# Performance work log

Hardware: AMD Instinct MI355X
Metric: run time of the kernel (lower is better)

The kernel has to match this reference:

```python
import jax, jax.numpy as jnp
import numpy as np

B, S, D, H, E, K = 2, 1024, 768, 12, 8, 2
DF = 4 * D
HD = D // H
EPS = 1e-5

def layer_norm(x, g, b):
    m = jnp.mean(x, axis=-1, keepdims=True)
    v = jnp.mean(jnp.square(x - m), axis=-1, keepdims=True)
    return (x - m) * jax.lax.rsqrt(v + EPS) * g + b

def setup_inputs() -> dict:
    key = jax.random.key(0)
    ks = jax.random.split(key, 16)
    s = lambda i, shape, sc: jax.random.normal(ks[i], shape, jnp.float32) * sc
    return {
        'x': s(0, (B, S, D), 1.0),
        'ln1_g': jnp.ones((D,), jnp.float32), 'ln1_b': jnp.zeros((D,), jnp.float32),
        'Wq': s(1, (D, D), 0.02), 'Wk': s(2, (D, D), 0.02), 'Wv': s(3, (D, D), 0.02),
        'Wo': s(4, (D, D), 0.02), 'bo': jnp.zeros((D,), jnp.float32),
        'ln2_g': jnp.ones((D,), jnp.float32), 'ln2_b': jnp.zeros((D,), jnp.float32),
        'Wr': s(5, (D, E), 0.02), 'br': jnp.zeros((E,), jnp.float32),
        'W1': s(6, (E, D, DF), 0.02), 'b1': jnp.zeros((E, DF), jnp.float32),
        'W2': s(7, (E, DF, D), 0.02), 'b2': jnp.zeros((E, D), jnp.float32),
    }

def _attn(xn, Wq, Wk, Wv, Wo, bo):
    # xn: [B,S,D]
    q = (xn @ Wq).reshape(B, S, H, HD).transpose(0, 2, 1, 3)
    k = (xn @ Wk).reshape(B, S, H, HD).transpose(0, 2, 1, 3)
    v = (xn @ Wv).reshape(B, S, H, HD).transpose(0, 2, 1, 3)
    scores = jnp.einsum('bhqd,bhkd->bhqk', q, k) / jnp.sqrt(jnp.float32(HD))
    causal = jnp.tril(jnp.ones((S, S), bool))
    scores = jnp.where(causal, scores, jnp.float32(-1e9))
    w = jax.nn.softmax(scores, axis=-1)
    out = jnp.einsum('bhqk,bhkd->bhqd', w, v)
    out = out.transpose(0, 2, 1, 3).reshape(B, S, D)
    return out @ Wo + bo

def _smoe(xn, Wr, br, W1, b1, W2, b2):
    logits = xn @ Wr + br                               # [B,S,E]
    topv, topi = jax.lax.top_k(logits, K)               # [B,S,K]
    gw = jax.nn.softmax(topv, axis=-1)                  # softmax over selected experts
    oh = jax.nn.one_hot(topi, E, dtype=xn.dtype)        # [B,S,K,E]
    gate = jnp.einsum('bske,bsk->bse', oh, gw)          # sparse gate, zeros elsewhere
    h = jax.nn.gelu(jnp.einsum('bsd,edf->bsef', xn, W1) + b1, approximate=False)
    eo = jnp.einsum('bsef,efd->bsed', h, W2) + b2       # [B,S,E,D]
    return jnp.einsum('bsed,bse->bsd', eo, gate)

def reference(x, ln1_g, ln1_b, Wq, Wk, Wv, Wo, bo, ln2_g, ln2_b, Wr, br, W1, b1, W2, b2):
    h = x + _attn(layer_norm(x, ln1_g, ln1_b), Wq, Wk, Wv, Wo, bo)
    out = h + _smoe(layer_norm(h, ln2_g, ln2_b), Wr, br, W1, b1, W2, b2)
    return out
```

## Files before the change

### kernel.cpp

```cpp
#include <hip/hip_runtime.h>

using bf16x8 = __attribute__((ext_vector_type(8))) short;
using bf16x4 = __attribute__((ext_vector_type(4))) short;
using f32x4  = __attribute__((ext_vector_type(4))) float;

#define DEV __device__ __forceinline__

DEV short f2bf(float x){
  unsigned u = __float_as_uint(x);
  u += 0x7fffu + ((u >> 16) & 1u);
  return (short)(u >> 16);
}
DEV float bf2f(short h){ return __uint_as_float(((unsigned)(unsigned short)h) << 16); }

#define MFMA16(a,b,c) __builtin_amdgcn_mfma_f32_16x16x32_bf16(a,b,c,0,0,0)

DEV void gl_lds16(const void* g, void* l){
  __builtin_amdgcn_global_load_lds(
      (const __attribute__((address_space(1))) unsigned*)g,
      (__attribute__((address_space(3))) unsigned*)l, 16, 0, 0);
}


__global__ void k_transpose(const float* __restrict__ src, long sbatch,
                            short* __restrict__ dhi, short* __restrict__ dlo, long dbatch,
                            int R, int C){
  __shared__ float tile[64][65];
  const float* s = src + (long)blockIdx.z * sbatch;
  int c0 = blockIdx.x * 64, r0 = blockIdx.y * 64;
  int tx = threadIdx.x & 15, ty = threadIdx.x >> 4;
  #pragma unroll
  for (int i = 0; i < 4; i++){
    int r = ty + 16*i;
    float4 v = *(const float4*)&s[(long)(r0 + r) * C + c0 + tx*4];
    tile[r][tx*4+0] = v.x; tile[r][tx*4+1] = v.y;
    tile[r][tx*4+2] = v.z; tile[r][tx*4+3] = v.w;
  }
  __syncthreads();
  int rseg = (threadIdx.x & 7) * 8;
  #pragma unroll
  for (int p = 0; p < 2; p++){
    int col = (threadIdx.x >> 3) + 32*p;
    short hv[8], lv[8];
    #pragma unroll
    for (int k = 0; k < 8; k++){
      float v = tile[rseg + k][col];
      hv[k] = f2bf(v);
      lv[k] = f2bf(v - bf2f(hv[k]));
    }
    long o = (long)blockIdx.z * dbatch + (long)(c0 + col) * R + r0 + rseg;
    *(bf16x8*)&dhi[o] = *(bf16x8*)&hv[0];
    if (dlo) *(bf16x8*)&dlo[o] = *(bf16x8*)&lv[0];
  }
}

__global__ void k_transpose4(const float* __restrict__ s0, const float* __restrict__ s1,
                             const float* __restrict__ s2, const float* __restrict__ s3,
                             short* __restrict__ d0h, short* __restrict__ d0l,
                             short* __restrict__ d1h, short* __restrict__ d1l,
                             short* __restrict__ d2h, short* __restrict__ d2l,
                             short* __restrict__ d3h, short* __restrict__ d3l){
  int z = blockIdx.z;
  const float* s = (z==0) ? s0 : (z==1) ? s1 : (z==2) ? s2 : s3;
  short* dh = (z==0) ? d0h : (z==1) ? d1h : (z==2) ? d2h : d3h;
  short* dl = (z==0) ? d0l : (z==1) ? d1l : (z==2) ? d2l : d3l;
  __shared__ float tile[64][65];
  int c0 = blockIdx.x * 64, r0 = blockIdx.y * 64;
  int tx = threadIdx.x & 15, ty = threadIdx.x >> 4;
  #pragma unroll
  for (int i = 0; i < 4; i++){
    int r = ty + 16*i;
    float4 v = *(const float4*)&s[(long)(r0 + r) * 768 + c0 + tx*4];
    tile[r][tx*4+0] = v.x; tile[r][tx*4+1] = v.y;
    tile[r][tx*4+2] = v.z; tile[r][tx*4+3] = v.w;
  }
  __syncthreads();
  int rseg = (threadIdx.x & 7) * 8;
  #pragma unroll
  for (int p = 0; p < 2; p++){
    int col = (threadIdx.x >> 3) + 32*p;
    short hv[8], lv[8];
    #pragma unroll
    for (int k = 0; k < 8; k++){
      float v = tile[rseg + k][col];
      hv[k] = f2bf(v);
      lv[k] = f2bf(v - bf2f(hv[k]));
    }
    long o = (long)(c0 + col) * 768 + r0 + rseg;
    *(bf16x8*)&dh[o] = *(bf16x8*)&hv[0];
    *(bf16x8*)&dl[o] = *(bf16x8*)&lv[0];
  }
}

__global__ void k_ln1(const float* __restrict__ x, const float* __restrict__ g,
                      const float* __restrict__ bb,
                      short* __restrict__ xh, short* __restrict__ xl){
  int t = blockIdx.x, tid = threadIdx.x;
  const float* xr = x + (long)t * 768;
  float v[3];
  #pragma unroll
  for (int j = 0; j < 3; j++) v[j] = xr[tid + 256*j];
  float s = v[0]+v[1]+v[2];
  float q = v[0]*v[0]+v[1]*v[1]+v[2]*v[2];
  #pragma unroll
  for (int o = 32; o > 0; o >>= 1){ s += __shfl_down(s,o,64); q += __shfl_down(q,o,64); }
  __shared__ float ss[4], qs[4];
  int w = tid >> 6;
  if ((tid & 63) == 0){ ss[w] = s; qs[w] = q; }
  __syncthreads();
  float St = ss[0]+ss[1]+ss[2]+ss[3], Qt = qs[0]+qs[1]+qs[2]+qs[3];
  float mean = St * (1.f/768.f);
  float var  = Qt * (1.f/768.f) - mean*mean;
  float inv  = 1.f / sqrtf(var + 1e-5f);
  #pragma unroll
  for (int j = 0; j < 3; j++){
    int d = tid + 256*j;
    float xn = (v[j]-mean)*inv*g[d] + bb[d];
    short hv = f2bf(xn);
    xh[(long)t*768 + d] = hv;
    xl[(long)t*768 + d] = f2bf(xn - bf2f(hv));
  }
}

__global__ __launch_bounds__(256,3) void k_qkv(
    const short* __restrict__ Ah, const short* __restrict__ Al,
    const short* __restrict__ Bh, const short* __restrict__ Bl,
    short* __restrict__ qh, short* __restrict__ ql,
    short* __restrict__ kh, short* __restrict__ kl,
    short* __restrict__ vh, short* __restrict__ vl){
  int M0 = blockIdx.x * 64, N0 = blockIdx.y * 128;
  __shared__ __align__(16) short lah[64*64], lal[64*64], lbh[128*64], lbl[128*64];
  int tid = threadIdx.x;
  int w = tid >> 6, lane = tid & 63, l15 = lane & 15, quad = lane >> 4;
  int mbase = (w & 1) * 32, nbase = (w >> 1) * 64;
  f32x4 acc[2][4];
  #pragma unroll
  for (int i = 0; i < 2; i++)
    #pragma unroll
    for (int j = 0; j < 4; j++) acc[i][j] = (f32x4){0.f,0.f,0.f,0.f};
  int rl = lane >> 3, pch = lane & 7;
  long gA[2], gB[4];
  #pragma unroll
  for (int j = 0; j < 2; j++){
    int r = w*16 + j*8 + rl;
    int c = pch ^ (r & 7);
    gA[j] = (long)(M0 + r)*768 + c*8;
  }
  #pragma unroll
  for (int j = 0; j < 4; j++){
    int r = w*32 + j*8 + rl;
    int c = pch ^ (r & 7);
    gB[j] = (long)(N0 + r)*768 + c*8;
  }
  for (int k0 = 0; k0 < 768; k0 += 64){
    #pragma unroll
    for (int j = 0; j < 2; j++){
      gl_lds16(Ah + gA[j] + k0, lah + w*1024 + j*512);
      gl_lds16(Al + gA[j] + k0, lal + w*1024 + j*512);
    }
    #pragma unroll
    for (int j = 0; j < 4; j++){
      gl_lds16(Bh + gB[j] + k0, lbh + w*2048 + j*512);
      gl_lds16(Bl + gB[j] + k0, lbl + w*2048 + j*512);
    }
    __syncthreads();
    #pragma unroll
    for (int kk = 0; kk < 2; kk++){
      int swq = ((kk*4 + quad) ^ (l15 & 7)) * 8;
      bf16x8 afh[2], afl[2];
      #pragma unroll
      for (int mt = 0; mt < 2; mt++){
        afh[mt] = *(const bf16x8*)&lah[(mbase+mt*16+l15)*64 + swq];
        afl[mt] = *(const bf16x8*)&lal[(mbase+mt*16+l15)*64 + swq];
      }
      #pragma unroll
      for (int nt = 0; nt < 4; nt++){
        bf16x8 bfh = *(const bf16x8*)&lbh[(nbase+nt*16+l15)*64 + swq];
        bf16x8 bfl = *(const bf16x8*)&lbl[(nbase+nt*16+l15)*64 + swq];
        #pragma unroll
        for (int mt = 0; mt < 2; mt++){
          acc[mt][nt] = MFMA16(afh[mt], bfh, acc[mt][nt]);
          acc[mt][nt] = MFMA16(afh[mt], bfl, acc[mt][nt]);
          acc[mt][nt] = MFMA16(afl[mt], bfh, acc[mt][nt]);
        }
      }
    }
    __syncthreads();
  }
  #pragma unroll
  for (int mt = 0; mt < 2; mt++){
    #pragma unroll
    for (int nt = 0; nt < 4; nt++){
      #pragma unroll
      for (int rg = 0; rg < 4; rg++){
        int m = M0 + mbase + mt*16 + quad*4 + rg;
        int n = N0 + nbase + nt*16 + l15;
        float vv = acc[mt][nt][rg];
        int bi = m >> 10, si = m & 1023;
        if (n < 768){
          float sv = vv * 0.18033688011112042f;
          short hv = f2bf(sv);
          int hh = n >> 6, hd = n & 63;
          long o = (((long)(bi*12+hh)*1024) + si)*64 + hd;
          qh[o] = hv; ql[o] = f2bf(sv - bf2f(hv));
        } else if (n < 1536){
          int n2 = n - 768;
          short hv = f2bf(vv);
          int hh = n2 >> 6, hd = n2 & 63;
          long o = (((long)(bi*12+hh)*1024) + si)*64 + hd;
          kh[o] = hv; kl[o] = f2bf(vv - bf2f(hv));
        } else {
          int n2 = n - 1536;
          short hv = f2bf(vv);
          int hh = n2 >> 6, hd = n2 & 63;
          long o = (((long)(bi*12+hh)*64) + hd)*1024 + si;
          vh[o] = hv; vl[o] = f2bf(vv - bf2f(hv));
        }
      }
    }
  }
}

__global__ __launch_bounds__(256,3) void k_attn(
    const short* __restrict__ qh, const short* __restrict__ ql,
    const short* __restrict__ kh, const short* __restrict__ kl,
    const short* __restrict__ vth, const short* __restrict__ vtl,
    float* __restrict__ po, float* __restrict__ pm, float* __restrict__ pl){
  int wid = (blockIdx.x + 3*blockIdx.y) & 31;
  int qt = wid >> 1, half = wid & 1, bh = blockIdx.y;
  int q0 = qt * 64;
  long base = (long)bh * 1024 * 64;
  int ktb = half ? ((qt + 2) >> 1) : 0;
  int kte = half ? (qt + 1) : ((qt + 2) >> 1);
  __shared__ __align__(16) short skh[64*64], skl[64*64], svh[64*64], svl[64*64];
  __shared__ __align__(16) short sph[4][16*72], spl[4][16*72];
  int tid = threadIdx.x, w = tid >> 6, lane = tid & 63, l15 = lane & 15, quad = lane >> 4;
  bf16x8 qfh[2], qfl[2];
  #pragma unroll
  for (int c = 0; c < 2; c++){
    long qa = base + (long)(q0 + w*16 + l15)*64 + c*32 + quad*8;
    qfh[c] = *(const bf16x8*)(qh + qa);
    qfl[c] = *(const bf16x8*)(ql + qa);
  }
  f32x4 oacc[4];
  #pragma unroll
  for (int i = 0; i < 4; i++) oacc[i] = (f32x4){0.f,0.f,0.f,0.f};
  float m_i[4] = {-1e30f,-1e30f,-1e30f,-1e30f};
  float l_i[4] = {0.f,0.f,0.f,0.f};
  const short* gsrc = (w==0) ? kh : (w==1) ? kl : (w==2) ? vth : vtl;
  short* myb = (w==0) ? skh : (w==1) ? skl : (w==2) ? svh : svl;
  bool isv = (w >= 2);
  int rloc = lane >> 3, pch = lane & 7;
  for (int kt = ktb; kt < kte; kt++){
    #pragma unroll
    for (int j = 0; j < 8; j++){
      int r = j*8 + rloc;
      int c = pch ^ (r & 7);
      long ga = isv ? (base + (long)r*1024 + kt*64 + c*8)
                    : (base + (long)(kt*64 + r)*64 + c*8);
      gl_lds16(gsrc + ga, myb + j*512);
    }
    __syncthreads();
    f32x4 sfr[4];
    #pragma unroll
    for (int nt = 0; nt < 4; nt++){
      f32x4 c = (f32x4){0.f,0.f,0.f,0.f};
      int krow = (nt*16 + l15) * 64;
      #pragma unroll
      for (int ch = 0; ch < 2; ch++){
        int pc = ((ch*4 + quad) ^ (l15 & 7)) * 8;
        bf16x8 kfh = *(const bf16x8*)&skh[krow + pc];
        bf16x8 kfl = *(const bf16x8*)&skl[krow + pc];
        c = MFMA16(qfh[ch], kfh, c);
        c = MFMA16(qfh[ch], kfl, c);
        c = MFMA16(qfl[ch], kfh, c);
      }
      sfr[nt] = c;
    }
    if (kt == qt){
      #pragma unroll
      for (int nt = 0; nt < 4; nt++)
        #pragma unroll
        for (int rg = 0; rg < 4; rg++){
          int kp = nt*16 + l15, qp = w*16 + quad*4 + rg;
          if (kp > qp) sfr[nt][rg] = -1e30f;
        }
    }
    float rmax[4];
    #pragma unroll
    for (int rg = 0; rg < 4; rg++)
      rmax[rg] = fmaxf(fmaxf(sfr[0][rg], sfr[1][rg]), fmaxf(sfr[2][rg], sfr[3][rg]));
    #pragma unroll
    for (int xm = 1; xm < 16; xm <<= 1)
      #pragma unroll
      for (int rg = 0; rg < 4; rg++)
        rmax[rg] = fmaxf(rmax[rg], __shfl_xor(rmax[rg], xm, 64));
    float alpha[4];
    #pragma unroll
    for (int rg = 0; rg < 4; rg++){
      float mn = fmaxf(m_i[rg], rmax[rg]);
      alpha[rg] = exp2f(m_i[rg] - mn);
      m_i[rg] = mn;
    }
    float rsum[4] = {0.f,0.f,0.f,0.f};
    #pragma unroll
    for (int nt = 0; nt < 4; nt++)
      #pragma unroll
      for (int rg = 0; rg < 4; rg++){
        float p = exp2f(sfr[nt][rg] - m_i[rg]);
        sfr[nt][rg] = p; rsum[rg] += p;
      }
    #pragma unroll
    for (int xm = 1; xm < 16; xm <<= 1)
      #pragma unroll
      for (int rg = 0; rg < 4; rg++)
        rsum[rg] += __shfl_xor(rsum[rg], xm, 64);
    #pragma unroll
    for (int rg = 0; rg < 4; rg++) l_i[rg] = l_i[rg]*alpha[rg] + rsum[rg];
    #pragma unroll
    for (int hd = 0; hd < 4; hd++)
      #pragma unroll
      for (int rg = 0; rg < 4; rg++) oacc[hd][rg] *= alpha[rg];
    #pragma unroll
    for (int nt = 0; nt < 4; nt++)
      #pragma unroll
      for (int rg = 0; rg < 4; rg++){
        float p = sfr[nt][rg];
        short hv = f2bf(p);
        sph[w][(quad*4+rg)*72 + nt*16 + l15] = hv;
        spl[w][(quad*4+rg)*72 + nt*16 + l15] = f2bf(p - bf2f(hv));
      }
    bf16x8 pfh[2], pfl[2];
    #pragma unroll
    for (int ch = 0; ch < 2; ch++){
      pfh[ch] = *(const bf16x8*)&sph[w][l15*72 + ch*32 + quad*8];
      pfl[ch] = *(const bf16x8*)&spl[w][l15*72 + ch*32 + quad*8];
    }
    #pragma unroll
    for (int hd = 0; hd < 4; hd++){
      int vrow = (hd*16 + l15) * 64;
      #pragma unroll
      for (int ch = 0; ch < 2; ch++){
        int pc = ((ch*4 + quad) ^ (l15 & 7)) * 8;
        bf16x8 vfh = *(const bf16x8*)&svh[vrow + pc];
        bf16x8 vfl = *(const bf16x8*)&svl[vrow + pc];
        oacc[hd] = MFMA16(pfh[ch], vfh, oacc[hd]);
        oacc[hd] = MFMA16(pfh[ch], vfl, oacc[hd]);
        oacc[hd] = MFMA16(pfl[ch], vfh, oacc[hd]);
      }
    }
    __syncthreads();
  }
  long pb = ((long)(half*24 + bh)*1024);
  #pragma unroll
  for (int hdt = 0; hdt < 4; hdt++)
    #pragma unroll
    for (int rg = 0; rg < 4; rg++){
      int qp = q0 + w*16 + quad*4 + rg;
      po[(pb + qp)*64 + hdt*16 + l15] = oacc[hdt][rg];
    }
  if (l15 == 0){
    #pragma unroll
    for (int rg = 0; rg < 4; rg++){
      int qp = q0 + w*16 + quad*4 + rg;
      pm[pb + qp] = m_i[rg];
      pl[pb + qp] = l_i[rg];
    }
  }
}

__global__ void k_attn_combine(const float* __restrict__ po, const float* __restrict__ pm,
                               const float* __restrict__ pl,
                               short* __restrict__ oh, short* __restrict__ ol){
  int bh = blockIdx.y, tid = threadIdx.x;
  int r = blockIdx.x*64 + (tid >> 2);
  int c0 = (tid & 3) * 16;
  long i0 = (long)bh*1024 + r;
  long i1 = (long)(24 + bh)*1024 + r;
  float m0 = pm[i0], m1 = pm[i1], l0 = pl[i0], l1 = pl[i1];
  float m = fmaxf(m0, m1);
  float a0 = exp2f(m0 - m), a1 = exp2f(m1 - m);
  float inv = 1.f / (a0*l0 + a1*l1);
  a0 *= inv; a1 *= inv;
  int b = bh / 12, hh = bh % 12;
  long ob = ((long)(b*1024 + r))*768 + hh*64 + c0;
  short hv[16], lv[16];
  #pragma unroll
  for (int j = 0; j < 4; j++){
    float4 o0 = *(const float4*)&po[i0*64 + c0 + j*4];
    float4 o1 = *(const float4*)&po[i1*64 + c0 + j*4];
    float vs[4] = {a0*o0.x + a1*o1.x, a0*o0.y + a1*o1.y,
                   a0*o0.z + a1*o1.z, a0*o0.w + a1*o1.w};
    #pragma unroll
    for (int q = 0; q < 4; q++){
      short h = f2bf(vs[q]);
      hv[j*4+q] = h; lv[j*4+q] = f2bf(vs[q] - bf2f(h));
    }
  }
  *(bf16x8*)(oh + ob)     = *(bf16x8*)&hv[0];
  *(bf16x8*)(oh + ob + 8) = *(bf16x8*)&hv[8];
  *(bf16x8*)(ol + ob)     = *(bf16x8*)&lv[0];
  *(bf16x8*)(ol + ob + 8) = *(bf16x8*)&lv[8];
}

__global__ __launch_bounds__(256,3) void k_wo(
    const short* __restrict__ Ah, const short* __restrict__ Al,
    const short* __restrict__ Bh, const short* __restrict__ Bl,
    float* __restrict__ p0, float* __restrict__ p1){
  int M0 = blockIdx.x * 64, N0 = blockIdx.y * 128;
  int ks = blockIdx.z;
  int kbeg = ks * 384;
  float* wp = ks ? p1 : p0;
  __shared__ __align__(16) short lah[64*64], lal[64*64], lbh[128*64], lbl[128*64];
  int tid = threadIdx.x;
  int w = tid >> 6, lane = tid & 63, l15 = lane & 15, quad = lane >> 4;
  int mbase = (w & 1) * 32, nbase = (w >> 1) * 64;
  f32x4 acc[2][4];
  #pragma unroll
  for (int i = 0; i < 2; i++)
    #pragma unroll
    for (int j = 0; j < 4; j++) acc[i][j] = (f32x4){0.f,0.f,0.f,0.f};
  int rl = lane >> 3, pch = lane & 7;
  long gA[2], gB[4];
  #pragma unroll
  for (int j = 0; j < 2; j++){
    int r = w*16 + j*8 + rl;
    int c = pch ^ (r & 7);
    gA[j] = (long)(M0 + r)*768 + kbeg + c*8;
  }
  #pragma unroll
  for (int j = 0; j < 4; j++){
    int r = w*32 + j*8 + rl;
    int c = pch ^ (r & 7);
    gB[j] = (long)(N0 + r)*768 + kbeg + c*8;
  }
  for (int k0 = 0; k0 < 384; k0 += 64){
    #pragma unroll
    for (int j = 0; j < 2; j++){
      gl_lds16(Ah + gA[j] + k0, lah + w*1024 + j*512);
      gl_lds16(Al + gA[j] + k0, lal + w*1024 + j*512);
    }
    #pragma unroll
    for (int j = 0; j < 4; j++){
      gl_lds16(Bh + gB[j] + k0, lbh + w*2048 + j*512);
      gl_lds16(Bl + gB[j] + k0, lbl + w*2048 + j*512);
    }
    __syncthreads();
    #pragma unroll
    for (int kk = 0; kk < 2; kk++){
      int swq = ((kk*4 + quad) ^ (l15 & 7)) * 8;
      bf16x8 afh[2], afl[2];
      #pragma unroll
      for (int mt = 0; mt < 2; mt++){
        afh[mt] = *(const bf16x8*)&lah[(mbase+mt*16+l15)*64 + swq];
        afl[mt] = *(const bf16x8*)&lal[(mbase+mt*16+l15)*64 + swq];
      }
      #pragma unroll
      for (int nt = 0; nt < 4; nt++){
        bf16x8 bfh = *(const bf16x8*)&lbh[(nbase+nt*16+l15)*64 + swq];
        bf16x8 bfl = *(const bf16x8*)&lbl[(nbase+nt*16+l15)*64 + swq];
        #pragma unroll
        for (int mt = 0; mt < 2; mt++){
          acc[mt][nt] = MFMA16(afh[mt], bfh, acc[mt][nt]);
          acc[mt][nt] = MFMA16(afh[mt], bfl, acc[mt][nt]);
          acc[mt][nt] = MFMA16(afl[mt], bfh, acc[mt][nt]);
        }
      }
    }
    __syncthreads();
  }
  #pragma unroll
  for (int mt = 0; mt < 2; mt++)
    #pragma unroll
    for (int nt = 0; nt < 4; nt++)
      #pragma unroll
      for (int rg = 0; rg < 4; rg++){
        int m = M0 + mbase + mt*16 + quad*4 + rg;
        int n = N0 + nbase + nt*16 + l15;
        wp[(long)m*768 + n] = acc[mt][nt][rg];
      }
}

__global__ void k_ln2router(const float* __restrict__ p0, const float* __restrict__ p1,
                            const float* __restrict__ x, const float* __restrict__ bo,
                            const float* __restrict__ g, const float* __restrict__ bb,
                            const float* __restrict__ Wr, const float* __restrict__ br,
                            float* __restrict__ hout, short* __restrict__ xn2,
                            int* __restrict__ sel, float* __restrict__ gw){
  int wv = (blockIdx.x*256 + threadIdx.x) >> 6;
  int lane = threadIdx.x & 63;
  #pragma unroll
  for (int rep = 0; rep < 2; rep++){
    int t = wv*2 + rep;
    float4 hv[3];
    #pragma unroll
    for (int j = 0; j < 3; j++){
      long i = (long)t*192 + j*64 + lane;
      float4 a  = ((const float4*)p0)[i];
      float4 b  = ((const float4*)p1)[i];
      float4 xx = ((const float4*)x)[i];
      float4 bv = ((const float4*)bo)[j*64 + lane];
      float4 h;
      h.x = a.x + b.x + xx.x + bv.x;
      h.y = a.y + b.y + xx.y + bv.y;
      h.z = a.z + b.z + xx.z + bv.z;
      h.w = a.w + b.w + xx.w + bv.w;
      ((float4*)hout)[i] = h;
      hv[j] = h;
    }
    float s = 0.f, q = 0.f;
    #pragma unroll
    for (int j = 0; j < 3; j++){
      s += hv[j].x + hv[j].y + hv[j].z + hv[j].w;
      q += hv[j].x*hv[j].x + hv[j].y*hv[j].y + hv[j].z*hv[j].z + hv[j].w*hv[j].w;
    }
    #pragma unroll
    for (int xm = 1; xm < 64; xm <<= 1){ s += __shfl_xor(s, xm, 64); q += __shfl_xor(q, xm, 64); }
    float mean = s * (1.f/768.f);
    float var  = q * (1.f/768.f) - mean*mean;
    float inv  = 1.f / sqrtf(var + 1e-5f);
    float part[8] = {0,0,0,0,0,0,0,0};
    #pragma unroll
    for (int j = 0; j < 3; j++){
      int d0 = (j*64 + lane) * 4;
      float4 gv = ((const float4*)g)[j*64 + lane];
      float4 bbv = ((const float4*)bb)[j*64 + lane];
      float xn0 = (hv[j].x - mean)*inv*gv.x + bbv.x;
      float xn1 = (hv[j].y - mean)*inv*gv.y + bbv.y;
      float xn2v = (hv[j].z - mean)*inv*gv.z + bbv.z;
      float xn3 = (hv[j].w - mean)*inv*gv.w + bbv.w;
      bf16x4 pk = (bf16x4){f2bf(xn0), f2bf(xn1), f2bf(xn2v), f2bf(xn3)};
      *(bf16x4*)&xn2[(long)t*768 + d0] = pk;
      #pragma unroll
      for (int e = 0; e < 8; e++){
        part[e] += xn0 * Wr[(d0+0)*8 + e];
        part[e] += xn1 * Wr[(d0+1)*8 + e];
        part[e] += xn2v * Wr[(d0+2)*8 + e];
        part[e] += xn3 * Wr[(d0+3)*8 + e];
      }
    }
    #pragma unroll
    for (int xm = 1; xm < 64; xm <<= 1)
      #pragma unroll
      for (int e = 0; e < 8; e++) part[e] += __shfl_xor(part[e], xm, 64);
    if (lane == 0){
      float lg[8];
      #pragma unroll
      for (int e = 0; e < 8; e++) lg[e] = part[e] + br[e];
      int i1 = 0;
      for (int e = 1; e < 8; e++) if (lg[e] > lg[i1]) i1 = e;
      int i2 = -1;
      for (int e = 0; e < 8; e++){ if (e == i1) continue; if (i2 < 0 || lg[e] > lg[i2]) i2 = e; }
      float e2 = expf(lg[i2] - lg[i1]);
      float is = 1.f / (1.f + e2);
      gw[t*2]   = is;
      gw[t*2+1] = e2 * is;
      sel[t*2]   = i1;
      sel[t*2+1] = i2;
    }
  }
}

__global__ void k_build(const int* __restrict__ sel, int* __restrict__ poffs,
                        int* __restrict__ mbc, int* __restrict__ ptot,
                        int* __restrict__ pperm, int* __restrict__ inv){
  __shared__ int cnt8[8], cur[8], wbase[16][8];
  int tid = threadIdx.x;
  int lane = tid & 63, wv = tid >> 6;
  if (tid < 8) cnt8[tid] = 0;
  __syncthreads();
  int sv[4];
  #pragma unroll
  for (int r = 0; r < 4; r++){
    sv[r] = sel[tid + r*1024];
    #pragma unroll
    for (int e = 0; e < 8; e++){
      unsigned long long mk = __ballot(sv[r] == e);
      if (lane == 0) atomicAdd(&cnt8[e], (int)__popcll(mk));
    }
  }
  __syncthreads();
  if (tid == 0){
    int p = 0;
    for (int e = 0; e < 8; e++){
      cur[e] = p; poffs[e] = p;
      int pc = (cnt8[e] + 127) & ~127;
      mbc[e] = pc >> 7;
      p += pc;
    }
    *ptot = p;
  }
  __syncthreads();
  #pragma unroll
  for (int r = 0; r < 5; r++) pperm[tid + r*1024] = -1;
  __syncthreads();
  unsigned long long lmask = (1ull << lane) - 1ull;
  #pragma unroll
  for (int r = 0; r < 4; r++){
    int s = sv[r];
    unsigned long long mk[8];
    #pragma unroll
    for (int e = 0; e < 8; e++) mk[e] = __ballot(s == e);
    if (lane == 0){
      #pragma unroll
      for (int e = 0; e < 8; e++)
        wbase[wv][e] = atomicAdd(&cur[e], (int)__popcll(mk[e]));
    }
    unsigned long long mks = 0;
    #pragma unroll
    for (int e = 0; e < 8; e++) if (s == e) mks = mk[e];
    int pos = wbase[wv][s] + (int)__popcll(mks & lmask);
    int i = tid + r*1024;
    pperm[pos] = i;
    inv[i] = pos;
  }
}

__global__ __launch_bounds__(256,3) void k_moe1(
    const short* __restrict__ xn2, const short* __restrict__ W1T,
    const float* __restrict__ b1,
    const int* __restrict__ poffs, const int* __restrict__ mbc,
    const int* __restrict__ pperm, short* __restrict__ h1){
  int t = blockIdx.x;
  int e = t / 24, n = t % 24;
  if ((int)blockIdx.y >= mbc[e]) return;
  int M0 = poffs[e] + blockIdx.y * 128;
  int N0 = n * 128;
  const short* Bp = W1T + (long)e * 3072 * 768;
  __shared__ __align__(16) short la[128*64], lb[128*64];
  __shared__ int rtok[128];
  int tid = threadIdx.x, w = tid >> 6, lane = tid & 63, l15 = lane & 15, quad = lane >> 4;
  if (tid < 128) rtok[tid] = pperm[M0 + tid];
  __syncthreads();
  int rl = lane >> 3, pch = lane & 7;
  long gA[4], gB[4];
  #pragma unroll
  for (int j = 0; j < 4; j++){
    int r = w*32 + j*8 + rl;
    int c = pch ^ (r & 7);
    int tk = rtok[r]; tk = (tk >= 0) ? (tk >> 1) : 0;
    gA[j] = (long)tk*768 + c*8;
    gB[j] = (long)(N0 + r)*768 + c*8;
  }
  short* ldA = la + w*2048;
  short* ldB = lb + w*2048;
  f32x4 acc[4][4];
  #pragma unroll
  for (int i = 0; i < 4; i++)
    #pragma unroll
    for (int j = 0; j < 4; j++) acc[i][j] = (f32x4){0.f,0.f,0.f,0.f};
  int mbase = (w & 1) * 64, nbase = (w >> 1) * 64;
  for (int k0 = 0; k0 < 768; k0 += 64){
    #pragma unroll
    for (int j = 0; j < 4; j++) gl_lds16(xn2 + gA[j] + k0, ldA + j*512);
    #pragma unroll
    for (int j = 0; j < 4; j++) gl_lds16(Bp  + gB[j] + k0, ldB + j*512);
    __syncthreads();
    #pragma unroll
    for (int kk = 0; kk < 2; kk++){
      int swq = ((kk*4 + quad) ^ (l15 & 7)) * 8;
      bf16x8 af[4];
      #pragma unroll
      for (int mt = 0; mt < 4; mt++)
        af[mt] = *(const bf16x8*)&la[(mbase+mt*16+l15)*64 + swq];
      #pragma unroll
      for (int nt = 0; nt < 4; nt++){
        bf16x8 bf = *(const bf16x8*)&lb[(nbase+nt*16+l15)*64 + swq];
        #pragma unroll
        for (int mt = 0; mt < 4; mt++) acc[mt][nt] = MFMA16(af[mt], bf, acc[mt][nt]);
      }
    }
    __syncthreads();
  }
  #pragma unroll
  for (int mt = 0; mt < 4; mt++)
    #pragma unroll
    for (int nt = 0; nt < 4; nt++)
      #pragma unroll
      for (int rg = 0; rg < 4; rg++){
        int ml = mbase + mt*16 + quad*4 + rg;
        if (rtok[ml] >= 0){
          int nn = N0 + nbase + nt*16 + l15;
          float vv = acc[mt][nt][rg] + b1[e*3072 + nn];
          float gl = 0.5f * vv * (1.f + erff(vv * 0.70710678118654752f));
          h1[(long)(M0 + ml)*3072 + nn] = f2bf(gl);
        }
      }
}

__global__ __launch_bounds__(256,4) void k_moe2(
    const short* __restrict__ h1, const short* __restrict__ W2T,
    const float* __restrict__ b2,
    const int* __restrict__ poffs, const int* __restrict__ mbc,
    float* __restrict__ e0, float* __restrict__ e1,
    float* __restrict__ e2, float* __restrict__ e3){
  int t = blockIdx.x;
  int e = t / 24, r24 = t % 24;
  int n = r24 >> 2, ks = r24 & 3;
  if ((int)blockIdx.y >= mbc[e]) return;
  int M0 = poffs[e] + blockIdx.y * 128;
  int N0 = n * 128;
  int kbeg = ks * 768;
  const short* Bp = W2T + (long)e * 768 * 3072;
  float* eo = (ks == 0) ? e0 : (ks == 1) ? e1 : (ks == 2) ? e2 : e3;
  __shared__ __align__(16) short la[128*64], lb[128*64];
  int tid = threadIdx.x, w = tid >> 6, lane = tid & 63, l15 = lane & 15, quad = lane >> 4;
  int rl = lane >> 3, pch = lane & 7;
  long gA[4], gB[4];
  #pragma unroll
  for (int j = 0; j < 4; j++){
    int r = w*32 + j*8 + rl;
    int c = pch ^ (r & 7);
    gA[j] = (long)(M0 + r)*3072 + kbeg + c*8;
    gB[j] = (long)(N0 + r)*3072 + kbeg + c*8;
  }
  short* ldA = la + w*2048;
  short* ldB = lb + w*2048;
  f32x4 acc[4][4];
  #pragma unroll
  for (int i = 0; i < 4; i++)
    #pragma unroll
    for (int j = 0; j < 4; j++) acc[i][j] = (f32x4){0.f,0.f,0.f,0.f};
  int mbase = (w & 1) * 64, nbase = (w >> 1) * 64;
  for (int k0 = 0; k0 < 768; k0 += 64){
    #pragma unroll
    for (int j = 0; j < 4; j++) gl_lds16(h1 + gA[j] + k0, ldA + j*512);
    #pragma unroll
    for (int j = 0; j < 4; j++) gl_lds16(Bp + gB[j] + k0, ldB + j*512);
    __syncthreads();
    #pragma unroll
    for (int kk = 0; kk < 2; kk++){
      int swq = ((kk*4 + quad) ^ (l15 & 7)) * 8;
      bf16x8 af[4];
      #pragma unroll
      for (int mt = 0; mt < 4; mt++)
        af[mt] = *(const bf16x8*)&la[(mbase+mt*16+l15)*64 + swq];
      #pragma unroll
      for (int nt = 0; nt < 4; nt++){
        bf16x8 bf = *(const bf16x8*)&lb[(nbase+nt*16+l15)*64 + swq];
        #pragma unroll
        for (int mt = 0; mt < 4; mt++) acc[mt][nt] = MFMA16(af[mt], bf, acc[mt][nt]);
      }
    }
    __syncthreads();
  }
  #pragma unroll
  for (int mt = 0; mt < 4; mt++)
    #pragma unroll
    for (int nt = 0; nt < 4; nt++)
      #pragma unroll
      for (int rg = 0; rg < 4; rg++){
        int ml = mbase + mt*16 + quad*4 + rg;
        int nn = N0 + nbase + nt*16 + l15;
        float vv = acc[mt][nt][rg] + ((ks == 0) ? b2[e*768 + nn] : 0.f);
        eo[(long)(M0 + ml)*768 + nn] = vv;
      }
}

__global__ void k_combine(const float* __restrict__ h,
                          const float* __restrict__ e0, const float* __restrict__ e1,
                          const float* __restrict__ e2, const float* __restrict__ e3,
                          const int* __restrict__ inv, const float* __restrict__ gw,
                          float* __restrict__ out){
  int i = blockIdx.x * 256 + threadIdx.x;
  int t = i / 192, c = i - t * 192;
  int s0 = inv[2*t], s1 = inv[2*t+1];
  float g0 = gw[2*t], g1 = gw[2*t+1];
  float4 a  = ((const float4*)h)[i];
  long o0 = (long)s0*192 + c, o1 = (long)s1*192 + c;
  float4 x0 = ((const float4*)e0)[o0];
  float4 y0 = ((const float4*)e1)[o0];
  float4 z0 = ((const float4*)e2)[o0];
  float4 w0 = ((const float4*)e3)[o0];
  float4 x1 = ((const float4*)e0)[o1];
  float4 y1 = ((const float4*)e1)[o1];
  float4 z1 = ((const float4*)e2)[o1];
  float4 w1 = ((const float4*)e3)[o1];
  float4 o;
  o.x = a.x + g0*(x0.x + y0.x + z0.x + w0.x) + g1*(x1.x + y1.x + z1.x + w1.x);
  o.y = a.y + g0*(x0.y + y0.y + z0.y + w0.y) + g1*(x1.y + y1.y + z1.y + w1.y);
  o.z = a.z + g0*(x0.z + y0.z + z0.z + w0.z) + g1*(x1.z + y1.z + z1.z + w1.z);
  o.w = a.w + g0*(x0.w + y0.w + z0.w + w0.w) + g1*(x1.w + y1.w + z1.w + w1.w);
  ((float4*)out)[i] = o;
}

extern "C" void kernel_launch(void* const* d_in, const int* in_sizes, int n_in,
                              void* d_out, int out_size, void* d_ws, size_t ws_size,
                              hipStream_t stream){
  const float* x    = (const float*)d_in[0];
  const float* ln1g = (const float*)d_in[1];
  const float* ln1b = (const float*)d_in[2];
  const float* Wq   = (const float*)d_in[3];
  const float* Wk   = (const float*)d_in[4];
  const float* Wv   = (const float*)d_in[5];
  const float* Wo   = (const float*)d_in[6];
  const float* bo   = (const float*)d_in[7];
  const float* ln2g = (const float*)d_in[8];
  const float* ln2b = (const float*)d_in[9];
  const float* Wr   = (const float*)d_in[10];
  const float* br   = (const float*)d_in[11];
  const float* W1   = (const float*)d_in[12];
  const float* b1   = (const float*)d_in[13];
  const float* W2   = (const float*)d_in[14];
  const float* b2   = (const float*)d_in[15];

  char* ws = (char*)d_ws;
  size_t off = 0;
  auto alloc = [&](size_t bytes) -> void* {
    void* p = ws + off;
    off += (bytes + 255) & ~(size_t)255;
    return p;
  };
  short* WQKVH = (short*)alloc(2304l*768*2);
  short* WQKVL = (short*)alloc(2304l*768*2);
  short* WOH   = (short*)alloc(768l*768*2);
  short* WOL   = (short*)alloc(768l*768*2);
  short* W1T   = (short*)alloc(8l*3072*768*2);
  short* W2T   = (short*)alloc(8l*768*3072*2);
  short* XN1H  = (short*)alloc(2048l*768*2);
  short* XN1L  = (short*)alloc(2048l*768*2);
  short* QH    = (short*)alloc(2048l*768*2);
  short* QL    = (short*)alloc(2048l*768*2);
  short* KH    = (short*)alloc(2048l*768*2);
  short* KL    = (short*)alloc(2048l*768*2);
  short* VTH   = (short*)alloc(2048l*768*2);
  short* VTL   = (short*)alloc(2048l*768*2);
  short* ATH   = (short*)alloc(2048l*768*2);
  short* ATL   = (short*)alloc(2048l*768*2);
  float* HBUF  = (float*)alloc(2048l*768*4);
  short* XN2   = (short*)alloc(2048l*768*2);
  short* H1    = (short*)alloc(5120l*3072*2);
  float* E0    = (float*)alloc(5120l*768*4);
  float* E1    = (float*)alloc(5120l*768*4);
  float* PO    = (float*)alloc(2l*24*1024*64*4);
  float* PM    = (float*)alloc(2l*24*1024*4);
  float* PL    = (float*)alloc(2l*24*1024*4);
  int*   POFF  = (int*)alloc(8*4);
  int*   MBC   = (int*)alloc(8*4);
  int*   PTOT  = (int*)alloc(4);
  int*   SEL   = (int*)alloc(4096*4);
  int*   PPERM = (int*)alloc(5120*4);
  int*   INV   = (int*)alloc(4096*4);
  float* GW    = (float*)alloc(4096*4);
  (void)ws_size; (void)in_sizes; (void)n_in; (void)out_size;

  float* E2 = (float*)XN1H;
  float* E3 = E2 + 5120l*768;
  float* WP0 = PO;
  float* WP1 = PO + 2048l*768;

  k_transpose4<<<dim3(12,12,4),256,0,stream>>>(
      Wq, Wk, Wv, Wo,
      WQKVH,             WQKVL,
      WQKVH + 768l*768,  WQKVL + 768l*768,
      WQKVH + 1536l*768, WQKVL + 1536l*768,
      WOH, WOL);
  k_transpose<<<dim3(48,12,8),256,0,stream>>>(W1, 768l*3072, W1T, nullptr, 3072l*768, 768, 3072);
  k_transpose<<<dim3(12,48,8),256,0,stream>>>(W2, 3072l*768, W2T, nullptr, 768l*3072, 3072, 768);

  k_ln1<<<2048,256,0,stream>>>(x, ln1g, ln1b, XN1H, XN1L);
  k_qkv<<<dim3(32,18),256,0,stream>>>(XN1H, XN1L, WQKVH, WQKVL, QH, QL, KH, KL, VTH, VTL);
  k_attn<<<dim3(32,24),256,0,stream>>>(QH, QL, KH, KL, VTH, VTL, PO, PM, PL);
  k_attn_combine<<<dim3(16,24),256,0,stream>>>(PO, PM, PL, ATH, ATL);
  k_wo<<<dim3(32,6,2),256,0,stream>>>(ATH, ATL, WOH, WOL, WP0, WP1);

  k_ln2router<<<256,256,0,stream>>>(WP0, WP1, x, bo, ln2g, ln2b, Wr, br,
                                    HBUF, XN2, SEL, GW);
  k_build<<<1,1024,0,stream>>>(SEL, POFF, MBC, PTOT, PPERM, INV);
  k_moe1<<<dim3(192,16),256,0,stream>>>(XN2, W1T, b1, POFF, MBC, PPERM, H1);
  k_moe2<<<dim3(192,16),256,0,stream>>>(H1, W2T, b2, POFF, MBC, E0, E1, E2, E3);
  k_combine<<<1536,256,0,stream>>>(HBUF, E0, E1, E2, E3, INV, GW, (float*)d_out);
}
```

Baseline: 436.5 us.

## Double-buffer LDS tiles in second MoE expert GEMM to overlap loads with MFMA

```diff
diff --git a/kernel.cpp b/kernel.cpp
--- a/kernel.cpp
+++ b/kernel.cpp
@@ -688,7 +688,7 @@
       }
 }
 
-__global__ __launch_bounds__(256,4) void k_moe2(
+__global__ __launch_bounds__(256,2) void k_moe2(
     const short* __restrict__ h1, const short* __restrict__ W2T,
     const float* __restrict__ b2,
     const int* __restrict__ poffs, const int* __restrict__ mbc,
@@ -703,7 +703,7 @@
   int kbeg = ks * 768;
   const short* Bp = W2T + (long)e * 768 * 3072;
   float* eo = (ks == 0) ? e0 : (ks == 1) ? e1 : (ks == 2) ? e2 : e3;
-  __shared__ __align__(16) short la[128*64], lb[128*64];
+  __shared__ __align__(16) short la[2][128*64], lb[2][128*64];
   int tid = threadIdx.x, w = tid >> 6, lane = tid & 63, l15 = lane & 15, quad = lane >> 4;
   int rl = lane >> 3, pch = lane & 7;
   long gA[4], gB[4];
@@ -714,35 +714,49 @@
     gA[j] = (long)(M0 + r)*3072 + kbeg + c*8;
     gB[j] = (long)(N0 + r)*3072 + kbeg + c*8;
   }
-  short* ldA = la + w*2048;
-  short* ldB = lb + w*2048;
   f32x4 acc[4][4];
   #pragma unroll
   for (int i = 0; i < 4; i++)
     #pragma unroll
     for (int j = 0; j < 4; j++) acc[i][j] = (f32x4){0.f,0.f,0.f,0.f};
   int mbase = (w & 1) * 64, nbase = (w >> 1) * 64;
-  for (int k0 = 0; k0 < 768; k0 += 64){
-    #pragma unroll
-    for (int j = 0; j < 4; j++) gl_lds16(h1 + gA[j] + k0, ldA + j*512);
-    #pragma unroll
-    for (int j = 0; j < 4; j++) gl_lds16(Bp + gB[j] + k0, ldB + j*512);
-    __syncthreads();
+  #pragma unroll
+  for (int j = 0; j < 4; j++){
+    gl_lds16(h1 + gA[j], &la[0][w*2048 + j*512]);
+    gl_lds16(Bp + gB[j], &lb[0][w*2048 + j*512]);
+  }
+  for (int st = 0; st < 12; st++){
+    int cur = st & 1;
+    if (st + 1 < 12){
+      #pragma unroll
+      for (int j = 0; j < 4; j++){
+        gl_lds16(h1 + gA[j] + (st+1)*64, &la[cur^1][w*2048 + j*512]);
+        gl_lds16(Bp + gB[j] + (st+1)*64, &lb[cur^1][w*2048 + j*512]);
+      }
+      asm volatile("s_waitcnt vmcnt(8)" ::: "memory");
+    } else {
+      asm volatile("s_waitcnt vmcnt(0)" ::: "memory");
+    }
+    __builtin_amdgcn_sched_barrier(0);
+    __builtin_amdgcn_s_barrier();
+    __builtin_amdgcn_sched_barrier(0);
     #pragma unroll
     for (int kk = 0; kk < 2; kk++){
       int swq = ((kk*4 + quad) ^ (l15 & 7)) * 8;
       bf16x8 af[4];
       #pragma unroll
       for (int mt = 0; mt < 4; mt++)
-        af[mt] = *(const bf16x8*)&la[(mbase+mt*16+l15)*64 + swq];
+        af[mt] = *(const bf16x8*)&la[cur][(mbase+mt*16+l15)*64 + swq];
       #pragma unroll
       for (int nt = 0; nt < 4; nt++){
-        bf16x8 bf = *(const bf16x8*)&lb[(nbase+nt*16+l15)*64 + swq];
+        bf16x8 bf = *(const bf16x8*)&lb[cur][(nbase+nt*16+l15)*64 + swq];
         #pragma unroll
         for (int mt = 0; mt < 4; mt++) acc[mt][nt] = MFMA16(af[mt], bf, acc[mt][nt]);
       }
     }
-    __syncthreads();
+    __builtin_amdgcn_sched_barrier(0);
+    __builtin_amdgcn_s_barrier();
+    __builtin_amdgcn_sched_barrier(0);
   }
   #pragma unroll
   for (int mt = 0; mt < 4; mt++)
```

Result: slower. 513.0 us (+17.5%).
